# Kernel optimization log

Hardware: AMD Instinct MI355X
Metric: run time of the kernel (lower is better)

The kernel has to match this reference:

```python
import jax, jax.numpy as jnp
import numpy as np

N, E = 50000, 800000
IN_DIM, H, OUT = 16, 256, 64
L = 3
REL_DIM, ROLE_DIM, COL_DIM = 16, 8, 8
NUM_REL, NUM_ROLE, NUM_COL = 8, 8, 3
EDGE_IN = 2 * H + REL_DIM + 2 * ROLE_DIM + 2 * COL_DIM   # 560
NODE_IN = 2 * H + ROLE_DIM + COL_DIM                     # 528
LN_EPS = 1e-5


def setup_inputs() -> dict:
    key = jax.random.key(0)
    ks = jax.random.split(key, 32)
    s = 0.02
    inp = {
        "scalars": jax.random.normal(ks[0], (N, IN_DIM), jnp.float32),
        "edge_index": jax.random.randint(ks[1], (2, E), 0, N),
        "edge_relation": jax.random.randint(ks[2], (E,), 0, NUM_REL),
        "node_color_rep": jax.random.randint(ks[3], (N,), 0, NUM_COL),
        "node_role": jax.random.randint(ks[4], (N,), 0, NUM_ROLE),
        # block-level embeddings + input projection (weights stored [in,out])
        "blk_role_emb": jax.random.normal(ks[5], (NUM_ROLE, 8), jnp.float32) * s,
        "blk_color_emb": jax.random.normal(ks[6], (NUM_COL, 8), jnp.float32) * s,
        "in_w": jax.random.normal(ks[7], (IN_DIM + 16, H), jnp.float32) * s,
        "in_b": jnp.zeros((H,), jnp.float32),
        # per-layer params, stacked over L
        "rel_embs": jax.random.normal(ks[8], (L, NUM_REL, REL_DIM), jnp.float32) * s,
        "role_embs": jax.random.normal(ks[9], (L, NUM_ROLE, ROLE_DIM), jnp.float32) * s,
        "col_embs": jax.random.normal(ks[10], (L, NUM_COL, COL_DIM), jnp.float32) * s,
        "e1_w": jax.random.normal(ks[11], (L, EDGE_IN, H), jnp.float32) * s,
        "e1_b": jnp.zeros((L, H), jnp.float32),
        "e2_w": jax.random.normal(ks[12], (L, H, H), jnp.float32) * s,
        "e2_b": jnp.zeros((L, H), jnp.float32),
        "n1_w": jax.random.normal(ks[13], (L, NODE_IN, H), jnp.float32) * s,
        "n1_b": jnp.zeros((L, H), jnp.float32),
        "n2_w": jax.random.normal(ks[14], (L, H, H), jnp.float32) * s,
        "n2_b": jnp.zeros((L, H), jnp.float32),
        "ln_g": jnp.ones((L, H), jnp.float32),
        "ln_b": jnp.zeros((L, H), jnp.float32),
        "out_w": jax.random.normal(ks[15], (H, OUT), jnp.float32) * s,
        "out_b": jnp.zeros((OUT,), jnp.float32),
    }
    return inp


def _layer(h, edge_index, edge_relation, node_color_rep, node_role,
           rel_e, role_e, col_e, e1w, e1b, e2w, e2b, n1w, n1b, n2w, n2b, g, b):
    src, dst = edge_index[0], edge_index[1]
    role_all = role_e[node_role]           # [N, ROLE_DIM]
    col_all = col_e[node_color_rep]        # [N, COL_DIM]
    edge_in = jnp.concatenate(
        [h[src], h[dst], rel_e[edge_relation],
         role_all[src], role_all[dst], col_all[src], col_all[dst]], axis=-1)
    m = jax.nn.silu(edge_in @ e1w + e1b)
    m = jax.nn.silu(m @ e2w + e2b)                       # [E, H]
    agg = jax.ops.segment_sum(m, dst, num_segments=h.shape[0])
    node_in = jnp.concatenate([h, agg, role_all, col_all], axis=-1)
    upd = jax.nn.silu(node_in @ n1w + n1b) @ n2w + n2b
    x = h + upd
    mu = jnp.mean(x, axis=-1, keepdims=True)
    var = jnp.mean(jnp.square(x - mu), axis=-1, keepdims=True)
    return g * (x - mu) * jax.lax.rsqrt(var + LN_EPS) + b


def reference(scalars, edge_index, edge_relation, node_color_rep, node_role,
              blk_role_emb, blk_color_emb, in_w, in_b,
              rel_embs, role_embs, col_embs,
              e1_w, e1_b, e2_w, e2_b, n1_w, n1_b, n2_w, n2_b,
              ln_g, ln_b, out_w, out_b):
    node_in = jnp.concatenate(
        [scalars, blk_color_emb[node_color_rep], blk_role_emb[node_role]], axis=-1)
    h = node_in @ in_w + in_b
    for i in range(L):
        h = _layer(h, edge_index, edge_relation, node_color_rep, node_role,
                   rel_embs[i], role_embs[i], col_embs[i],
                   e1_w[i], e1_b[i], e2_w[i], e2_b[i],
                   n1_w[i], n1_b[i], n2_w[i], n2_b[i],
                   ln_g[i], ln_b[i])
    return h @ out_w + out_b
```

## Files before the change

### kernel.cpp

```cpp
#include <hip/hip_runtime.h>

#define NN 50000
#define NE 800000
#define H 256
#define NB (NE / 64)
#define NBINS 50176

typedef __bf16 bf16x8 __attribute__((ext_vector_type(8)));
typedef __bf16 bf16x4 __attribute__((ext_vector_type(4)));
typedef float f32x4 __attribute__((ext_vector_type(4)));

static __device__ __forceinline__ f32x4 mfma16(bf16x8 a, bf16x8 b, f32x4 c) {
  return __builtin_amdgcn_mfma_f32_16x16x32_bf16(a, b, c, 0, 0, 0);
}
static __device__ __forceinline__ bf16x8 bzero8() {
  bf16x8 z;
#pragma unroll
  for (int j = 0; j < 8; ++j) z[j] = (__bf16)0.f;
  return z;
}
static __device__ __forceinline__ float silu_f(float v) {
  return v * __builtin_amdgcn_rcpf(1.f + __builtin_amdgcn_exp2f(v * -1.442695041f));
}
static __device__ __forceinline__ void add4(float4& a, const float4 b) {
  a.x += b.x; a.y += b.y; a.z += b.z; a.w += b.w;
}

__global__ void prep_kernel(
    const float* __restrict__ e1w, const float* __restrict__ e2w,
    const float* __restrict__ n1w, const float* __restrict__ n2w,
    const float* __restrict__ outw, const float* __restrict__ e1b,
    const float* __restrict__ rel_embs, const float* __restrict__ role_embs,
    const float* __restrict__ col_embs,
    __bf16* __restrict__ wsd, __bf16* __restrict__ e2p,
    __bf16* __restrict__ n1p, __bf16* __restrict__ n2p,
    __bf16* __restrict__ outp, int* __restrict__ cnt,
    float* __restrict__ TR, float* __restrict__ TS, float* __restrict__ TD)
{
  int i = blockIdx.x * 256 + threadIdx.x;
  if (i < 3 * 131072) {
    const int l = i / 131072, rem = i % 131072;
    const int c = rem >> 14, r2 = rem & 16383;
    const int n = r2 >> 5, k = c * 32 + (r2 & 31);
    wsd[i] = (n < 256) ? (__bf16)e1w[((size_t)l * 560 + k) * 256 + n]
                       : (__bf16)e1w[((size_t)l * 560 + 256 + k) * 256 + (n - 256)];
    return;
  }
  i -= 3 * 131072;
  if (i < 3 * 65536) {
    const int l = i / 65536, rem = i % 65536;
    const int c = rem >> 13, r2 = rem & 8191;
    const int n = r2 >> 5, k = c * 32 + (r2 & 31);
    e2p[i] = (__bf16)e2w[((size_t)l * 256 + k) * 256 + n];
    return;
  }
  i -= 3 * 65536;
  if (i < 3 * 139264) {
    const int l = i / 139264, rem = i % 139264;
    const int c = rem >> 13, r2 = rem & 8191;
    const int n = r2 >> 5, k = c * 32 + (r2 & 31);
    n1p[i] = (k < 528) ? (__bf16)n1w[((size_t)l * 528 + k) * 256 + n] : (__bf16)0.f;
    return;
  }
  i -= 3 * 139264;
  if (i < 3 * 65536) {
    const int l = i / 65536, rem = i % 65536;
    const int c = rem >> 13, r2 = rem & 8191;
    const int n = r2 >> 5, k = c * 32 + (r2 & 31);
    n2p[i] = (__bf16)n2w[((size_t)l * 256 + k) * 256 + n];
    return;
  }
  i -= 3 * 65536;
  if (i < 16384) {
    const int c = i >> 11, r2 = i & 2047;
    const int n = r2 >> 5, k = c * 32 + (r2 & 31);
    outp[i] = (__bf16)outw[(size_t)k * 64 + n];
    return;
  }
  i -= 16384;
  if (i < NBINS) { cnt[i] = 0; return; }
  i -= NBINS;
  if (i < 768) {
    const int l = i >> 8, c = i & 255;
    float w[48];
#pragma unroll
    for (int j = 0; j < 48; ++j) w[j] = e1w[((size_t)l * 560 + 512 + j) * 256 + c];
#pragma unroll
    for (int r = 0; r < 8; ++r) {
      float s = 0.f;
#pragma unroll
      for (int j = 0; j < 16; ++j) s += rel_embs[l * 128 + r * 16 + j] * w[j];
      TR[((size_t)l * 8 + r) * 256 + c] = s;
    }
    const float bias = e1b[l * 256 + c];
#pragma unroll
    for (int ro = 0; ro < 8; ++ro) {
      float ss = 0.f, sd = 0.f;
#pragma unroll
      for (int j = 0; j < 8; ++j) {
        ss += role_embs[l * 64 + ro * 8 + j] * w[16 + j];
        sd += role_embs[l * 64 + ro * 8 + j] * w[24 + j];
      }
#pragma unroll
      for (int co = 0; co < 3; ++co) {
        float cs = 0.f, cd = 0.f;
#pragma unroll
        for (int j = 0; j < 8; ++j) {
          cs += col_embs[l * 24 + co * 8 + j] * w[32 + j];
          cd += col_embs[l * 24 + co * 8 + j] * w[40 + j];
        }
        TS[((size_t)l * 24 + ro * 3 + co) * 256 + c] = ss + cs;
        TD[((size_t)l * 24 + ro * 3 + co) * 256 + c] = sd + cd + bias;
      }
    }
  }
}

__global__ void hist_kernel(const int* __restrict__ dstI, int* __restrict__ cnt) {
  const int e = blockIdx.x * 256 + threadIdx.x;
  if (e < NE) atomicAdd(&cnt[dstI[e]], 1);
}

__global__ __launch_bounds__(1024) void scan_kernel(int* __restrict__ cnt) {
  __shared__ int wsum[16];
  __shared__ int carry;
  const int tid = threadIdx.x, lane = tid & 63, wid = tid >> 6;
  if (tid == 0) carry = 0;
  __syncthreads();
  for (int base = 0; base < NBINS; base += 4096) {
    const int idx = base + tid * 4;
    int4 v = make_int4(0, 0, 0, 0);
    if (idx < NBINS) v = *(const int4*)&cnt[idx];
    const int s1 = v.x + v.y, s2 = s1 + v.z, tot = s2 + v.w;
    int x = tot;
#pragma unroll
    for (int d = 1; d < 64; d <<= 1) {
      const int y = __shfl_up(x, d, 64);
      if (lane >= d) x += y;
    }
    if (lane == 63) wsum[wid] = x;
    __syncthreads();
    int wpref = 0;
#pragma unroll
    for (int w = 0; w < 16; ++w)
      if (w < wid) wpref += wsum[w];
    const int ex = carry + wpref + (x - tot);
    if (idx < NBINS) {
      int4 o;
      o.x = ex; o.y = ex + v.x; o.z = ex + s1; o.w = ex + s2;
      *(int4*)&cnt[idx] = o;
    }
    __syncthreads();
    if (tid == 0) {
      int s = 0;
#pragma unroll
      for (int w = 0; w < 16; ++w) s += wsum[w];
      carry += s;
    }
    __syncthreads();
  }
}

__global__ void scatter_kernel(const int* __restrict__ srcI, const int* __restrict__ dstI,
                               const int* __restrict__ erel, int* __restrict__ cnt,
                               int* __restrict__ esr, int* __restrict__ dstS) {
  const int e = blockIdx.x * 256 + threadIdx.x;
  if (e < NE) {
    const int d = dstI[e];
    const int pos = atomicAdd(&cnt[d], 1);
    esr[pos] = srcI[e] | (erel[e] << 16);
    dstS[pos] = d;
  }
}

__global__ __launch_bounds__(256) void embed_kernel(
    const float* __restrict__ scalars, const int* __restrict__ ncol,
    const int* __restrict__ nrole,
    const float* __restrict__ colEmb, const float* __restrict__ roleEmb,
    const float* __restrict__ inw, const float* __restrict__ inb,
    __bf16* __restrict__ h)
{
  __shared__ float sW[32][256];
  __shared__ float sIn[16][32];
  const int tid = threadIdx.x;
  const int n0 = blockIdx.x * 16;
#pragma unroll
  for (int j = 0; j < 32; ++j) sW[j][tid] = inw[j * 256 + tid];
  {
    const int node = tid >> 4, k = tid & 15;
    const int n = n0 + node;
    sIn[node][k] = (n < NN) ? scalars[(size_t)n * 16 + k] : 0.f;
  }
  if (tid < 16) {
    const int n = n0 + tid;
    if (n < NN) {
      const int c = ncol[n], r = nrole[n];
#pragma unroll
      for (int j = 0; j < 8; ++j) {
        sIn[tid][16 + j] = colEmb[c * 8 + j];
        sIn[tid][24 + j] = roleEmb[r * 8 + j];
      }
    } else {
#pragma unroll
      for (int j = 0; j < 16; ++j) sIn[tid][16 + j] = 0.f;
    }
  }
  __syncthreads();
  const float bias = inb[tid];
  for (int nn = 0; nn < 16; ++nn) {
    const int n = n0 + nn;
    if (n >= NN) break;
    float acc = bias;
#pragma unroll
    for (int k = 0; k < 32; ++k) acc += sIn[nn][k] * sW[k][tid];
    h[(size_t)n * H + tid] = (__bf16)acc;
  }
}

__global__ __launch_bounds__(256, 4) void pre_kernel(
    const __bf16* __restrict__ h, const int* __restrict__ nrole,
    const int* __restrict__ ncol, const __bf16* __restrict__ wsd,
    const float* __restrict__ TS, const float* __restrict__ TD,
    __bf16* __restrict__ PS, __bf16* __restrict__ PD)
{
  __shared__ __align__(16) __bf16 Ah[64][72];
  const int tid  = threadIdx.x;
  const int lane = tid & 63;
  const int wave = tid >> 6;
  const int l15  = lane & 15;
  const int quad = lane >> 4;
  const int n0   = (blockIdx.x >> 1) * 64;
  const int half = blockIdx.x & 1;
  const int colW = wave * 64;

  f32x4 acc[4][4] = {};
  for (int s = 0; s < 4; ++s) {
    if (s) __syncthreads();
#pragma unroll
    for (int it = 0; it < 2; ++it) {
      const int t = tid + it * 256;
      const int row = t >> 3, seg = t & 7;
      const int n = n0 + row;
      bf16x8 v = bzero8();
      if (n < NN) v = *(const bf16x8*)(h + (size_t)n * H + s * 64 + seg * 8);
      *(bf16x8*)&Ah[row][seg * 8] = v;
    }
    __syncthreads();
#pragma unroll
    for (int cc = 0; cc < 2; ++cc) {
      const int c = 2 * s + cc;
      bf16x8 bfr[4], afr[4];
#pragma unroll
      for (int nj = 0; nj < 4; ++nj)
        bfr[nj] = *(const bf16x8*)(wsd + ((size_t)c * 512 + half * 256 + colW + nj * 16 + l15) * 32 + quad * 8);
#pragma unroll
      for (int mi = 0; mi < 4; ++mi)
        afr[mi] = *(const bf16x8*)&Ah[mi * 16 + l15][cc * 32 + quad * 8];
#pragma unroll
      for (int mi = 0; mi < 4; ++mi)
#pragma unroll
        for (int nj = 0; nj < 4; ++nj)
          acc[mi][nj] = mfma16(afr[mi], bfr[nj], acc[mi][nj]);
    }
  }

  const float* T = half ? TD : TS;
  __bf16* P = half ? PD : PS;
#pragma unroll
  for (int mi = 0; mi < 4; ++mi)
#pragma unroll
    for (int r = 0; r < 4; ++r) {
      const int n = n0 + mi * 16 + quad * 4 + r;
      if (n < NN) {
        const int ti = (nrole[n] * 3 + ncol[n]) * 256;
#pragma unroll
        for (int nj = 0; nj < 4; ++nj) {
          const int col = colW + nj * 16 + l15;
          P[(size_t)n * H + col] = (__bf16)(acc[mi][nj][r] + T[ti + col]);
        }
      }
    }
}

__global__ __launch_bounds__(256, 4) void edge_kernel(
    const __bf16* __restrict__ PS, const __bf16* __restrict__ PD,
    float* __restrict__ agg, float* __restrict__ bnd,
    const int* __restrict__ esr, const int* __restrict__ dstS,
    const float* __restrict__ TR,
    const __bf16* __restrict__ e2p, const float* __restrict__ e2b)
{
  __shared__ __align__(16) char uni[34816];
  __shared__ __bf16 sTrel[8][256];
  __shared__ int sSrc[64], sDst[64], sRel[64];

  auto A2  = (__bf16 (*)[264])uni;
  auto A2t = (__bf16 (*)[68])uni;

  const int tid  = threadIdx.x;
  const int lane = tid & 63;
  const int wave = tid >> 6;
  const int l15  = lane & 15;
  const int quad = lane >> 4;
  const int e0   = blockIdx.x * 64;
  const int colW = wave * 64;

  if (tid < 64) {
    const int u = esr[e0 + tid];
    sSrc[tid] = u & 0xffff;
    sRel[tid] = u >> 16;
    sDst[tid] = dstS[e0 + tid];
  }
  {
    const int r = tid >> 5, cs = (tid & 31) * 8;
    const float* p = TR + r * 256 + cs;
    bf16x8 v;
#pragma unroll
    for (int j = 0; j < 8; ++j) v[j] = (__bf16)p[j];
    *(bf16x8*)&sTrel[r][cs] = v;
  }
  __syncthreads();

  {
    const int brow = tid >> 5;
    const int cs = (tid & 31) * 8;
#pragma unroll
    for (int it = 0; it < 8; ++it) {
      const int row = it * 8 + brow;
      const bf16x8 a = *(const bf16x8*)(PS + (size_t)sSrc[row] * H + cs);
      const bf16x8 b = *(const bf16x8*)(PD + (size_t)sDst[row] * H + cs);
      const bf16x8 t = *(const bf16x8*)&sTrel[sRel[row]][cs];
      bf16x8 o;
#pragma unroll
      for (int j = 0; j < 8; ++j)
        o[j] = (__bf16)silu_f((float)a[j] + (float)b[j] + (float)t[j]);
      *(bf16x8*)&A2[row][cs] = o;
    }
  }
  __syncthreads();

  f32x4 acc2[4][4] = {};
#pragma unroll
  for (int c = 0; c < 8; ++c) {
    bf16x8 bfr[4], afr[4];
#pragma unroll
    for (int nj = 0; nj < 4; ++nj)
      bfr[nj] = *(const bf16x8*)(e2p + ((size_t)c * 256 + colW + nj * 16 + l15) * 32 + quad * 8);
#pragma unroll
    for (int mi = 0; mi < 4; ++mi)
      afr[mi] = *(const bf16x8*)&A2[mi * 16 + l15][c * 32 + quad * 8];
#pragma unroll
    for (int mi = 0; mi < 4; ++mi)
#pragma unroll
      for (int nj = 0; nj < 4; ++nj)
        acc2[mi][nj] = mfma16(afr[mi], bfr[nj], acc2[mi][nj]);
  }

  float b2[4];
#pragma unroll
  for (int nj = 0; nj < 4; ++nj) b2[nj] = e2b[colW + nj * 16 + l15];
  __syncthreads();

#pragma unroll
  for (int mi = 0; mi < 4; ++mi)
#pragma unroll
    for (int nj = 0; nj < 4; ++nj) {
      const int col = colW + nj * 16 + l15;
      bf16x4 pv;
#pragma unroll
      for (int r = 0; r < 4; ++r)
        pv[r] = (__bf16)silu_f(acc2[mi][nj][r] + b2[nj]);
      *(bf16x4*)&A2t[col][mi * 16 + quad * 4] = pv;
    }
  __syncthreads();

  {
    const int col = tid;
    const bool f = (lane > 0) && (sDst[lane] != sDst[lane - 1]);
    const unsigned long long mask = __ballot(f);
    bf16x4 v[16];
#pragma unroll
    for (int j = 0; j < 16; ++j) v[j] = *(const bf16x4*)&A2t[col][j * 4];
    float* bnd0 = bnd + ((size_t)2 * blockIdx.x) * 256 + col;
    float sum = 0.f;
    int s0 = 0;
#pragma unroll
    for (int r = 0; r < 64; ++r) {
      sum += (float)v[r >> 2][r & 3];
      if (r == 63 || ((mask >> (r + 1)) & 1ull)) {
        const bool isFirst = (s0 == 0), isLast = (r == 63);
        if (isFirst) {
          bnd0[0] = isLast ? 0.f : sum;
          if (isLast) bnd0[256] = sum;
        } else if (isLast) {
          bnd0[256] = sum;
        } else {
          agg[(size_t)sDst[r] * H + col] = sum;
        }
        sum = 0.f;
        s0 = r + 1;
      }
    }
  }
}

__global__ __launch_bounds__(256, 4) void node_kernel(
    __bf16* __restrict__ h, const float* __restrict__ agg,
    const float* __restrict__ bnd, const int* __restrict__ cnt,
    const int* __restrict__ nrole, const int* __restrict__ ncol,
    const float* __restrict__ roleE, const float* __restrict__ colE,
    const __bf16* __restrict__ n1p, const float* __restrict__ n1b,
    const __bf16* __restrict__ n2p, const float* __restrict__ n2b,
    const float* __restrict__ lng, const float* __restrict__ lnb,
    const int mode,
    const __bf16* __restrict__ wsdN, const float* __restrict__ TSn,
    const float* __restrict__ TDn, __bf16* __restrict__ PS, __bf16* __restrict__ PD,
    const __bf16* __restrict__ outp, const float* __restrict__ outb,
    float* __restrict__ out)
{
  __shared__ __align__(16) char uni[33792];
  __shared__ __bf16 sRole[8][8], sCol[3][8];
  __shared__ float sSum[64][4], sSsq[64][4];
  __shared__ int sStart[64], sEnd[64], sTi[64];

  auto Abuf = (__bf16 (*)[72])uni;
  auto A2   = (__bf16 (*)[264])uni;

  const int tid  = threadIdx.x;
  const int lane = tid & 63;
  const int wave = tid >> 6;
  const int l15  = lane & 15;
  const int quad = lane >> 4;
  const int n0   = blockIdx.x * 64;
  const int colW = wave * 64;

  if (tid < 64) {
    const int n = n0 + tid;
    int st = 0, en = 0, ti = 0;
    if (n < NN) {
      st = (n > 0) ? cnt[n - 1] : 0;
      en = cnt[n];
      ti = (nrole[n] * 3 + ncol[n]) * 256;
    }
    sStart[tid] = st; sEnd[tid] = en; sTi[tid] = ti;
    ((__bf16*)sRole)[tid] = (__bf16)roleE[tid];
  } else if (tid < 88) {
    ((__bf16*)sCol)[tid - 64] = (__bf16)colE[tid - 64];
  }
  __syncthreads();

  f32x4 acc[4][4] = {};
  for (int s = 0; s < 9; ++s) {
    if (s) __syncthreads();
    if (s < 4) {
#pragma unroll
      for (int it = 0; it < 2; ++it) {
        const int t = tid + it * 256;
        const int row = t >> 3, seg = t & 7;
        const int n = n0 + row;
        bf16x8 v = bzero8();
        if (n < NN) v = *(const bf16x8*)(h + (size_t)n * H + s * 64 + seg * 8);
        *(bf16x8*)&Abuf[row][seg * 8] = v;
      }
    } else if (s < 8) {
#pragma unroll
      for (int it = 0; it < 2; ++it) {
        const int t = tid + it * 256;
        const int row = t >> 3, seg = t & 7;
        const int off = (s - 4) * 64 + seg * 8;
        const int st = sStart[row], en = sEnd[row];
        float4 u0 = make_float4(0.f, 0.f, 0.f, 0.f);
        float4 u1 = make_float4(0.f, 0.f, 0.f, 0.f);
        if (en > st) {
          const int bs = st >> 6, be = (en - 1) >> 6;
          const bool interior = (bs == be) && (st & 63) != 0 && (en & 63) != 0;
          if (interior) {
            const float* p = agg + (size_t)(n0 + row) * H + off;
            u0 = *(const float4*)p;
            u1 = *(const float4*)(p + 4);
          } else {
            for (int b = bs; b <= be; ++b) {
              if (b > bs || (st & 63) == 0) {
                const float* p = bnd + ((size_t)2 * b) * 256 + off;
                add4(u0, *(const float4*)p);
                add4(u1, *(const float4*)(p + 4));
              }
              if (b < be || (en & 63) == 0) {
                const float* p = bnd + ((size_t)2 * b + 1) * 256 + off;
                add4(u0, *(const float4*)p);
                add4(u1, *(const float4*)(p + 4));
              }
            }
          }
        }
        bf16x8 v;
        v[0] = (__bf16)u0.x; v[1] = (__bf16)u0.y; v[2] = (__bf16)u0.z; v[3] = (__bf16)u0.w;
        v[4] = (__bf16)u1.x; v[5] = (__bf16)u1.y; v[6] = (__bf16)u1.z; v[7] = (__bf16)u1.w;
        *(bf16x8*)&Abuf[row][seg * 8] = v;
      }
    } else {
      const int row = tid >> 2, q = tid & 3;
      const int n = n0 + row;
      __bf16* dp = &Abuf[row][q * 16];
      if (q == 0 && n < NN) {
        const int r = nrole[n], c = ncol[n];
#pragma unroll
        for (int j = 0; j < 8; ++j) { dp[j] = sRole[r][j]; dp[8 + j] = sCol[c][j]; }
      } else {
#pragma unroll
        for (int j = 0; j < 16; ++j) dp[j] = (__bf16)0.f;
      }
    }
    __syncthreads();
#pragma unroll
    for (int cc = 0; cc < 2; ++cc) {
      const int c = 2 * s + cc;
      if (c >= 17) break;
      bf16x8 bfr[4], afr[4];
#pragma unroll
      for (int nj = 0; nj < 4; ++nj)
        bfr[nj] = *(const bf16x8*)(n1p + ((size_t)c * 256 + colW + nj * 16 + l15) * 32 + quad * 8);
#pragma unroll
      for (int mi = 0; mi < 4; ++mi)
        afr[mi] = *(const bf16x8*)&Abuf[mi * 16 + l15][cc * 32 + quad * 8];
#pragma unroll
      for (int mi = 0; mi < 4; ++mi)
#pragma unroll
        for (int nj = 0; nj < 4; ++nj)
          acc[mi][nj] = mfma16(afr[mi], bfr[nj], acc[mi][nj]);
    }
  }
  __syncthreads();

  float b1[4];
#pragma unroll
  for (int nj = 0; nj < 4; ++nj) b1[nj] = n1b[colW + nj * 16 + l15];
#pragma unroll
  for (int mi = 0; mi < 4; ++mi)
#pragma unroll
    for (int nj = 0; nj < 4; ++nj)
#pragma unroll
      for (int r = 0; r < 4; ++r)
        A2[mi * 16 + quad * 4 + r][colW + nj * 16 + l15] =
            (__bf16)silu_f(acc[mi][nj][r] + b1[nj]);
  __syncthreads();

  f32x4 acc2[4][4] = {};
#pragma unroll
  for (int c = 0; c < 8; ++c) {
    bf16x8 bfr[4], afr[4];
#pragma unroll
    for (int nj = 0; nj < 4; ++nj)
      bfr[nj] = *(const bf16x8*)(n2p + ((size_t)c * 256 + colW + nj * 16 + l15) * 32 + quad * 8);
#pragma unroll
    for (int mi = 0; mi < 4; ++mi)
      afr[mi] = *(const bf16x8*)&A2[mi * 16 + l15][c * 32 + quad * 8];
#pragma unroll
    for (int mi = 0; mi < 4; ++mi)
#pragma unroll
      for (int nj = 0; nj < 4; ++nj)
        acc2[mi][nj] = mfma16(afr[mi], bfr[nj], acc2[mi][nj]);
  }

  float b2[4], g4[4], bb4[4];
#pragma unroll
  for (int nj = 0; nj < 4; ++nj) {
    const int col = colW + nj * 16 + l15;
    b2[nj] = n2b[col]; g4[nj] = lng[col]; bb4[nj] = lnb[col];
  }
#pragma unroll
  for (int mi = 0; mi < 4; ++mi)
#pragma unroll
    for (int r = 0; r < 4; ++r) {
      const int n = n0 + mi * 16 + quad * 4 + r;
#pragma unroll
      for (int nj = 0; nj < 4; ++nj) {
        const float hv = (n < NN) ? (float)h[(size_t)n * H + colW + nj * 16 + l15] : 0.f;
        acc2[mi][nj][r] += b2[nj] + hv;
      }
    }
#pragma unroll
  for (int mi = 0; mi < 4; ++mi)
#pragma unroll
    for (int r = 0; r < 4; ++r) {
      float s1 = 0.f, s2 = 0.f;
#pragma unroll
      for (int nj = 0; nj < 4; ++nj) {
        const float v = acc2[mi][nj][r];
        s1 += v; s2 += v * v;
      }
#pragma unroll
      for (int d = 1; d < 16; d <<= 1) {
        s1 += __shfl_xor(s1, d, 16);
        s2 += __shfl_xor(s2, d, 16);
      }
      if (l15 == 0) {
        const int row = mi * 16 + quad * 4 + r;
        sSum[row][wave] = s1; sSsq[row][wave] = s2;
      }
    }
  __syncthreads();

#pragma unroll
  for (int mi = 0; mi < 4; ++mi)
#pragma unroll
    for (int r = 0; r < 4; ++r) {
      const int row = mi * 16 + quad * 4 + r;
      const int n = n0 + row;
      const float t1 = sSum[row][0] + sSum[row][1] + sSum[row][2] + sSum[row][3];
      const float t2 = sSsq[row][0] + sSsq[row][1] + sSsq[row][2] + sSsq[row][3];
      const float mu = t1 * (1.f / 256.f);
      float var = t2 * (1.f / 256.f) - mu * mu;
      var = var < 0.f ? 0.f : var;
      const float rstd = rsqrtf(var + 1e-5f);
#pragma unroll
      for (int nj = 0; nj < 4; ++nj) {
        const int col = colW + nj * 16 + l15;
        const float o = g4[nj] * (acc2[mi][nj][r] - mu) * rstd + bb4[nj];
        const __bf16 ob = (__bf16)o;
        A2[row][col] = ob;
        if (mode == 0 && n < NN) h[(size_t)n * H + col] = ob;
      }
    }
  __syncthreads();

  if (mode == 0) {
    for (int hf = 0; hf < 2; ++hf) {
      f32x4 ap[4][4] = {};
#pragma unroll
      for (int c = 0; c < 8; ++c) {
        bf16x8 bfr[4], afr[4];
#pragma unroll
        for (int nj = 0; nj < 4; ++nj)
          bfr[nj] = *(const bf16x8*)(wsdN + ((size_t)c * 512 + hf * 256 + colW + nj * 16 + l15) * 32 + quad * 8);
#pragma unroll
        for (int mi = 0; mi < 4; ++mi)
          afr[mi] = *(const bf16x8*)&A2[mi * 16 + l15][c * 32 + quad * 8];
#pragma unroll
        for (int mi = 0; mi < 4; ++mi)
#pragma unroll
          for (int nj = 0; nj < 4; ++nj)
            ap[mi][nj] = mfma16(afr[mi], bfr[nj], ap[mi][nj]);
      }
      const float* T = hf ? TDn : TSn;
      __bf16* P = hf ? PD : PS;
#pragma unroll
      for (int mi = 0; mi < 4; ++mi)
#pragma unroll
        for (int r = 0; r < 4; ++r) {
          const int row = mi * 16 + quad * 4 + r;
          const int n = n0 + row;
          if (n < NN) {
            const int ti = sTi[row];
#pragma unroll
            for (int nj = 0; nj < 4; ++nj) {
              const int col = colW + nj * 16 + l15;
              P[(size_t)n * H + col] = (__bf16)(ap[mi][nj][r] + T[ti + col]);
            }
          }
        }
    }
  } else {
    f32x4 ao[4] = {};
#pragma unroll
    for (int c = 0; c < 8; ++c) {
      const bf16x8 bfr = *(const bf16x8*)(outp + ((size_t)c * 64 + wave * 16 + l15) * 32 + quad * 8);
#pragma unroll
      for (int mi = 0; mi < 4; ++mi) {
        const bf16x8 afr = *(const bf16x8*)&A2[mi * 16 + l15][c * 32 + quad * 8];
        ao[mi] = mfma16(afr, bfr, ao[mi]);
      }
    }
    const float ob = outb[wave * 16 + l15];
#pragma unroll
    for (int mi = 0; mi < 4; ++mi)
#pragma unroll
      for (int r = 0; r < 4; ++r) {
        const int n = n0 + mi * 16 + quad * 4 + r;
        if (n < NN) out[(size_t)n * 64 + wave * 16 + l15] = ao[mi][r] + ob;
      }
  }
}

extern "C" void kernel_launch(void* const* d_in, const int* in_sizes, int n_in,
                              void* d_out, int out_size, void* d_ws, size_t ws_size,
                              hipStream_t stream) {
  const float* scalars   = (const float*)d_in[0];
  const int*   ei        = (const int*)d_in[1];
  const int*   erel      = (const int*)d_in[2];
  const int*   ncol      = (const int*)d_in[3];
  const int*   nrole     = (const int*)d_in[4];
  const float* blk_role  = (const float*)d_in[5];
  const float* blk_col   = (const float*)d_in[6];
  const float* inw       = (const float*)d_in[7];
  const float* inb       = (const float*)d_in[8];
  const float* rel_embs  = (const float*)d_in[9];
  const float* role_embs = (const float*)d_in[10];
  const float* col_embs  = (const float*)d_in[11];
  const float* e1w       = (const float*)d_in[12];
  const float* e1b       = (const float*)d_in[13];
  const float* e2w       = (const float*)d_in[14];
  const float* e2b       = (const float*)d_in[15];
  const float* n1w       = (const float*)d_in[16];
  const float* n1b       = (const float*)d_in[17];
  const float* n2w       = (const float*)d_in[18];
  const float* n2b       = (const float*)d_in[19];
  const float* lng       = (const float*)d_in[20];
  const float* lnb       = (const float*)d_in[21];
  const float* outw      = (const float*)d_in[22];
  const float* outb      = (const float*)d_in[23];

  const int* srcI = ei;
  const int* dstI = ei + NE;

  char* ws = (char*)d_ws;
  size_t off = 0;
  auto take = [&](size_t bytes) -> char* {
    off = (off + 255) & ~(size_t)255;
    char* p = ws + off;
    off += bytes;
    return p;
  };
  __bf16* h    = (__bf16*)take((size_t)NN * H * 2);
  float*  agg  = (float*)take((size_t)NN * H * 4);
  float*  bnd  = (float*)take((size_t)2 * NB * 256 * 4);
  __bf16* PS   = (__bf16*)take((size_t)NN * H * 2);
  __bf16* PD   = (__bf16*)take((size_t)NN * H * 2);
  __bf16* wsd  = (__bf16*)take((size_t)3 * 131072 * 2);
  __bf16* e2p  = (__bf16*)take((size_t)3 * 65536 * 2);
  __bf16* n1p  = (__bf16*)take((size_t)3 * 139264 * 2);
  __bf16* n2p  = (__bf16*)take((size_t)3 * 65536 * 2);
  __bf16* outp = (__bf16*)take((size_t)16384 * 2);
  float*  TR   = (float*)take((size_t)3 * 8 * 256 * 4);
  float*  TS   = (float*)take((size_t)3 * 24 * 256 * 4);
  float*  TD   = (float*)take((size_t)3 * 24 * 256 * 4);
  int*    cnt  = (int*)take((size_t)NBINS * 4);
  int*    esr  = (int*)take((size_t)NE * 4);
  int*    dstS = (int*)take((size_t)NE * 4);

  prep_kernel<<<4967, 256, 0, stream>>>(e1w, e2w, n1w, n2w, outw, e1b,
                                        rel_embs, role_embs, col_embs,
                                        wsd, e2p, n1p, n2p, outp, cnt, TR, TS, TD);
  hist_kernel<<<(NE + 255) / 256, 256, 0, stream>>>(dstI, cnt);
  scan_kernel<<<1, 1024, 0, stream>>>(cnt);
  scatter_kernel<<<(NE + 255) / 256, 256, 0, stream>>>(srcI, dstI, erel, cnt,
                                                       esr, dstS);
  embed_kernel<<<(NN + 15) / 16, 256, 0, stream>>>(scalars, ncol, nrole,
                                                   blk_col, blk_role, inw, inb, h);
  pre_kernel<<<2 * ((NN + 63) / 64), 256, 0, stream>>>(
      h, nrole, ncol, wsd, TS, TD, PS, PD);

  for (int l = 0; l < 3; ++l) {
    edge_kernel<<<NB, 256, 0, stream>>>(
        PS, PD, agg, bnd, esr, dstS, TR + (size_t)l * 2048,
        e2p + (size_t)l * 65536, e2b + (size_t)l * 256);
    const int mode = (l < 2) ? 0 : 1;
    node_kernel<<<(NN + 63) / 64, 256, 0, stream>>>(
        h, agg, bnd, cnt, nrole, ncol,
        role_embs + (size_t)l * 64, col_embs + (size_t)l * 24,
        n1p + (size_t)l * 139264, n1b + (size_t)l * 256,
        n2p + (size_t)l * 65536,  n2b + (size_t)l * 256,
        lng + (size_t)l * 256, lnb + (size_t)l * 256,
        mode,
        wsd + (size_t)(l + 1 < 3 ? l + 1 : 0) * 131072,
        TS + (size_t)(l + 1 < 3 ? l + 1 : 0) * 6144,
        TD + (size_t)(l + 1 < 3 ? l + 1 : 0) * 6144,
        PS, PD, outp, outb, (float*)d_out);
  }
}
```

Measured before the change: 1.308 ms.

## Merge setup kernels, fold node role/color embeddings into bias table, remap edge blocks

```diff
diff --git a/kernel.cpp b/kernel.cpp
--- a/kernel.cpp
+++ b/kernel.cpp
@@ -3,7 +3,7 @@
 #define NN 50000
 #define NE 800000
 #define H 256
-#define NB (NE / 64)
+#define NB 12500
 #define NBINS 50176
 
 typedef __bf16 bf16x8 __attribute__((ext_vector_type(8)));
@@ -26,17 +26,24 @@
   a.x += b.x; a.y += b.y; a.z += b.z; a.w += b.w;
 }
 
-__global__ void prep_kernel(
+__global__ void preph_kernel(
     const float* __restrict__ e1w, const float* __restrict__ e2w,
     const float* __restrict__ n1w, const float* __restrict__ n2w,
     const float* __restrict__ outw, const float* __restrict__ e1b,
+    const float* __restrict__ n1b,
     const float* __restrict__ rel_embs, const float* __restrict__ role_embs,
-    const float* __restrict__ col_embs,
+    const float* __restrict__ col_embs, const int* __restrict__ dstI,
     __bf16* __restrict__ wsd, __bf16* __restrict__ e2p,
     __bf16* __restrict__ n1p, __bf16* __restrict__ n2p,
     __bf16* __restrict__ outp, int* __restrict__ cnt,
-    float* __restrict__ TR, float* __restrict__ TS, float* __restrict__ TD)
+    float* __restrict__ TR, float* __restrict__ TS, float* __restrict__ TD,
+    float* __restrict__ TN)
 {
+  if (blockIdx.x >= 4675) {
+    const int e = (blockIdx.x - 4675) * 256 + threadIdx.x;
+    if (e < NE) atomicAdd(&cnt[dstI[e]], 1);
+    return;
+  }
   int i = blockIdx.x * 256 + threadIdx.x;
   if (i < 3 * 131072) {
     const int l = i / 131072, rem = i % 131072;
@@ -55,14 +62,14 @@
     return;
   }
   i -= 3 * 65536;
-  if (i < 3 * 139264) {
-    const int l = i / 139264, rem = i % 139264;
+  if (i < 3 * 131072) {
+    const int l = i / 131072, rem = i % 131072;
     const int c = rem >> 13, r2 = rem & 8191;
     const int n = r2 >> 5, k = c * 32 + (r2 & 31);
-    n1p[i] = (k < 528) ? (__bf16)n1w[((size_t)l * 528 + k) * 256 + n] : (__bf16)0.f;
+    n1p[i] = (__bf16)n1w[((size_t)l * 528 + k) * 256 + n];
     return;
   }
-  i -= 3 * 139264;
+  i -= 3 * 131072;
   if (i < 3 * 65536) {
     const int l = i / 65536, rem = i % 65536;
     const int c = rem >> 13, r2 = rem & 8191;
@@ -78,8 +85,6 @@
     return;
   }
   i -= 16384;
-  if (i < NBINS) { cnt[i] = 0; return; }
-  i -= NBINS;
   if (i < 768) {
     const int l = i >> 8, c = i & 255;
     float w[48];
@@ -92,33 +97,38 @@
       for (int j = 0; j < 16; ++j) s += rel_embs[l * 128 + r * 16 + j] * w[j];
       TR[((size_t)l * 8 + r) * 256 + c] = s;
     }
+    float wn[16];
+#pragma unroll
+    for (int j = 0; j < 16; ++j) wn[j] = n1w[((size_t)l * 528 + 512 + j) * 256 + c];
     const float bias = e1b[l * 256 + c];
+    const float nbias = n1b[l * 256 + c];
 #pragma unroll
     for (int ro = 0; ro < 8; ++ro) {
-      float ss = 0.f, sd = 0.f;
+      float ss = 0.f, sd = 0.f, sn = 0.f;
 #pragma unroll
       for (int j = 0; j < 8; ++j) {
-        ss += role_embs[l * 64 + ro * 8 + j] * w[16 + j];
-        sd += role_embs[l * 64 + ro * 8 + j] * w[24 + j];
+        const float re = role_embs[l * 64 + ro * 8 + j];
+        ss += re * w[16 + j];
+        sd += re * w[24 + j];
+        sn += re * wn[j];
       }
 #pragma unroll
       for (int co = 0; co < 3; ++co) {
-        float cs = 0.f, cd = 0.f;
+        float cs = 0.f, cd = 0.f, cn = 0.f;
 #pragma unroll
         for (int j = 0; j < 8; ++j) {
-          cs += col_embs[l * 24 + co * 8 + j] * w[32 + j];
-          cd += col_embs[l * 24 + co * 8 + j] * w[40 + j];
+          const float ce = col_embs[l * 24 + co * 8 + j];
+          cs += ce * w[32 + j];
+          cd += ce * w[40 + j];
+          cn += ce * wn[8 + j];
         }
-        TS[((size_t)l * 24 + ro * 3 + co) * 256 + c] = ss + cs;
-        TD[((size_t)l * 24 + ro * 3 + co) * 256 + c] = sd + cd + bias;
-      }
-    }
-  }
-}
-
-__global__ void hist_kernel(const int* __restrict__ dstI, int* __restrict__ cnt) {
-  const int e = blockIdx.x * 256 + threadIdx.x;
-  if (e < NE) atomicAdd(&cnt[dstI[e]], 1);
+        const size_t o = ((size_t)l * 24 + ro * 3 + co) * 256 + c;
+        TS[o] = ss + cs;
+        TD[o] = sd + cd + bias;
+        TN[o] = sn + cn + nbias;
+      }
+    }
+  }
 }
 
 __global__ __launch_bounds__(1024) void scan_kernel(int* __restrict__ cnt) {
@@ -161,125 +171,143 @@
   }
 }
 
-__global__ void scatter_kernel(const int* __restrict__ srcI, const int* __restrict__ dstI,
-                               const int* __restrict__ erel, int* __restrict__ cnt,
-                               int* __restrict__ esr, int* __restrict__ dstS) {
-  const int e = blockIdx.x * 256 + threadIdx.x;
-  if (e < NE) {
-    const int d = dstI[e];
-    const int pos = atomicAdd(&cnt[d], 1);
-    esr[pos] = srcI[e] | (erel[e] << 16);
-    dstS[pos] = d;
-  }
-}
-
-__global__ __launch_bounds__(256) void embed_kernel(
+__global__ __launch_bounds__(256, 4) void scem_kernel(
+    const int* __restrict__ srcI, const int* __restrict__ dstI,
+    const int* __restrict__ erel, int* __restrict__ cnt,
+    int* __restrict__ esr, int* __restrict__ dstS,
     const float* __restrict__ scalars, const int* __restrict__ ncol,
     const int* __restrict__ nrole,
     const float* __restrict__ colEmb, const float* __restrict__ roleEmb,
     const float* __restrict__ inw, const float* __restrict__ inb,
-    __bf16* __restrict__ h)
+    const __bf16* __restrict__ wsd,
+    const float* __restrict__ TS, const float* __restrict__ TD,
+    __bf16* __restrict__ h, __bf16* __restrict__ PS, __bf16* __restrict__ PD)
 {
-  __shared__ float sW[32][256];
-  __shared__ float sIn[16][32];
-  const int tid = threadIdx.x;
-  const int n0 = blockIdx.x * 16;
-#pragma unroll
-  for (int j = 0; j < 32; ++j) sW[j][tid] = inw[j * 256 + tid];
-  {
-    const int node = tid >> 4, k = tid & 15;
-    const int n = n0 + node;
-    sIn[node][k] = (n < NN) ? scalars[(size_t)n * 16 + k] : 0.f;
-  }
-  if (tid < 16) {
-    const int n = n0 + tid;
-    if (n < NN) {
-      const int c = ncol[n], r = nrole[n];
-#pragma unroll
-      for (int j = 0; j < 8; ++j) {
-        sIn[tid][16 + j] = colEmb[c * 8 + j];
-        sIn[tid][24 + j] = roleEmb[r * 8 + j];
-      }
-    } else {
-#pragma unroll
-      for (int j = 0; j < 16; ++j) sIn[tid][16 + j] = 0.f;
-    }
-  }
-  __syncthreads();
-  const float bias = inb[tid];
-  for (int nn = 0; nn < 16; ++nn) {
-    const int n = n0 + nn;
-    if (n >= NN) break;
-    float acc = bias;
-#pragma unroll
-    for (int k = 0; k < 32; ++k) acc += sIn[nn][k] * sW[k][tid];
-    h[(size_t)n * H + tid] = (__bf16)acc;
-  }
-}
-
-__global__ __launch_bounds__(256, 4) void pre_kernel(
-    const __bf16* __restrict__ h, const int* __restrict__ nrole,
-    const int* __restrict__ ncol, const __bf16* __restrict__ wsd,
-    const float* __restrict__ TS, const float* __restrict__ TD,
-    __bf16* __restrict__ PS, __bf16* __restrict__ PD)
-{
-  __shared__ __align__(16) __bf16 Ah[64][72];
+  if (blockIdx.x < 3125) {
+    const int e = blockIdx.x * 256 + threadIdx.x;
+    if (e < NE) {
+      const int d = dstI[e];
+      const int pos = atomicAdd(&cnt[d], 1);
+      esr[pos] = srcI[e] | (erel[e] << 16);
+      dstS[pos] = d;
+    }
+    return;
+  }
+  __shared__ __align__(16) char uni[34816];
+  __shared__ int sTi[64];
+  auto Ain = (__bf16 (*)[40])uni;
+  auto Hs  = (__bf16 (*)[264])uni;
+
   const int tid  = threadIdx.x;
   const int lane = tid & 63;
   const int wave = tid >> 6;
   const int l15  = lane & 15;
   const int quad = lane >> 4;
-  const int n0   = (blockIdx.x >> 1) * 64;
-  const int half = blockIdx.x & 1;
+  const int n0   = (blockIdx.x - 3125) * 64;
   const int colW = wave * 64;
 
+  if (tid < 64) {
+    const int n = n0 + tid;
+    sTi[tid] = (n < NN) ? (nrole[n] * 3 + ncol[n]) * 256 : 0;
+  }
+  {
+    const int row = tid >> 2, q = tid & 3;
+    const int n = n0 + row;
+    __bf16* dp = &Ain[row][q * 8];
+    if (n < NN) {
+      if (q < 2) {
+#pragma unroll
+        for (int j = 0; j < 8; ++j) dp[j] = (__bf16)scalars[(size_t)n * 16 + q * 8 + j];
+      } else if (q == 2) {
+        const int c = ncol[n];
+#pragma unroll
+        for (int j = 0; j < 8; ++j) dp[j] = (__bf16)colEmb[c * 8 + j];
+      } else {
+        const int r = nrole[n];
+#pragma unroll
+        for (int j = 0; j < 8; ++j) dp[j] = (__bf16)roleEmb[r * 8 + j];
+      }
+    } else {
+#pragma unroll
+      for (int j = 0; j < 8; ++j) dp[j] = (__bf16)0.f;
+    }
+  }
+  __syncthreads();
+
   f32x4 acc[4][4] = {};
-  for (int s = 0; s < 4; ++s) {
-    if (s) __syncthreads();
-#pragma unroll
-    for (int it = 0; it < 2; ++it) {
-      const int t = tid + it * 256;
-      const int row = t >> 3, seg = t & 7;
+  {
+    bf16x8 bfr[4], afr[4];
+#pragma unroll
+    for (int nj = 0; nj < 4; ++nj) {
+      const int col = colW + nj * 16 + l15;
+#pragma unroll
+      for (int j = 0; j < 8; ++j) bfr[nj][j] = (__bf16)inw[(quad * 8 + j) * 256 + col];
+    }
+#pragma unroll
+    for (int mi = 0; mi < 4; ++mi)
+      afr[mi] = *(const bf16x8*)&Ain[mi * 16 + l15][quad * 8];
+#pragma unroll
+    for (int mi = 0; mi < 4; ++mi)
+#pragma unroll
+      for (int nj = 0; nj < 4; ++nj)
+        acc[mi][nj] = mfma16(afr[mi], bfr[nj], acc[mi][nj]);
+  }
+  float bi[4];
+#pragma unroll
+  for (int nj = 0; nj < 4; ++nj) bi[nj] = inb[colW + nj * 16 + l15];
+  __syncthreads();
+
+#pragma unroll
+  for (int mi = 0; mi < 4; ++mi)
+#pragma unroll
+    for (int r = 0; r < 4; ++r) {
+      const int row = mi * 16 + quad * 4 + r;
       const int n = n0 + row;
-      bf16x8 v = bzero8();
-      if (n < NN) v = *(const bf16x8*)(h + (size_t)n * H + s * 64 + seg * 8);
-      *(bf16x8*)&Ah[row][seg * 8] = v;
-    }
-    __syncthreads();
-#pragma unroll
-    for (int cc = 0; cc < 2; ++cc) {
-      const int c = 2 * s + cc;
+#pragma unroll
+      for (int nj = 0; nj < 4; ++nj) {
+        const int col = colW + nj * 16 + l15;
+        const __bf16 hv = (__bf16)(acc[mi][nj][r] + bi[nj]);
+        Hs[row][col] = hv;
+        if (n < NN) h[(size_t)n * H + col] = hv;
+      }
+    }
+  __syncthreads();
+
+  for (int hf = 0; hf < 2; ++hf) {
+    f32x4 ap[4][4] = {};
+#pragma unroll
+    for (int c = 0; c < 8; ++c) {
       bf16x8 bfr[4], afr[4];
 #pragma unroll
       for (int nj = 0; nj < 4; ++nj)
-        bfr[nj] = *(const bf16x8*)(wsd + ((size_t)c * 512 + half * 256 + colW + nj * 16 + l15) * 32 + quad * 8);
+        bfr[nj] = *(const bf16x8*)(wsd + ((size_t)c * 512 + hf * 256 + colW + nj * 16 + l15) * 32 + quad * 8);
 #pragma unroll
       for (int mi = 0; mi < 4; ++mi)
-        afr[mi] = *(const bf16x8*)&Ah[mi * 16 + l15][cc * 32 + quad * 8];
+        afr[mi] = *(const bf16x8*)&Hs[mi * 16 + l15][c * 32 + quad * 8];
 #pragma unroll
       for (int mi = 0; mi < 4; ++mi)
 #pragma unroll
         for (int nj = 0; nj < 4; ++nj)
-          acc[mi][nj] = mfma16(afr[mi], bfr[nj], acc[mi][nj]);
-    }
-  }
-
-  const float* T = half ? TD : TS;
-  __bf16* P = half ? PD : PS;
-#pragma unroll
-  for (int mi = 0; mi < 4; ++mi)
-#pragma unroll
-    for (int r = 0; r < 4; ++r) {
-      const int n = n0 + mi * 16 + quad * 4 + r;
-      if (n < NN) {
-        const int ti = (nrole[n] * 3 + ncol[n]) * 256;
-#pragma unroll
-        for (int nj = 0; nj < 4; ++nj) {
-          const int col = colW + nj * 16 + l15;
-          P[(size_t)n * H + col] = (__bf16)(acc[mi][nj][r] + T[ti + col]);
+          ap[mi][nj] = mfma16(afr[mi], bfr[nj], ap[mi][nj]);
+    }
+    const float* T = hf ? TD : TS;
+    __bf16* P = hf ? PD : PS;
+#pragma unroll
+    for (int mi = 0; mi < 4; ++mi)
+#pragma unroll
+      for (int r = 0; r < 4; ++r) {
+        const int row = mi * 16 + quad * 4 + r;
+        const int n = n0 + row;
+        if (n < NN) {
+          const int ti = sTi[row];
+#pragma unroll
+          for (int nj = 0; nj < 4; ++nj) {
+            const int col = colW + nj * 16 + l15;
+            P[(size_t)n * H + col] = (__bf16)(ap[mi][nj][r] + T[ti + col]);
+          }
         }
       }
-    }
+  }
 }
 
 __global__ __launch_bounds__(256, 4) void edge_kernel(
@@ -289,6 +317,10 @@
     const float* __restrict__ TR,
     const __bf16* __restrict__ e2p, const float* __restrict__ e2b)
 {
+  const int g = blockIdx.x;
+  const int bb = (g & 7) * 1563 + (g >> 3);
+  if (bb >= NB) return;
+
   __shared__ __align__(16) char uni[34816];
   __shared__ __bf16 sTrel[8][256];
   __shared__ int sSrc[64], sDst[64], sRel[64];
@@ -301,7 +333,7 @@
   const int wave = tid >> 6;
   const int l15  = lane & 15;
   const int quad = lane >> 4;
-  const int e0   = blockIdx.x * 64;
+  const int e0   = bb * 64;
   const int colW = wave * 64;
 
   if (tid < 64) {
@@ -380,7 +412,7 @@
     bf16x4 v[16];
 #pragma unroll
     for (int j = 0; j < 16; ++j) v[j] = *(const bf16x4*)&A2t[col][j * 4];
-    float* bnd0 = bnd + ((size_t)2 * blockIdx.x) * 256 + col;
+    float* bnd0 = bnd + ((size_t)2 * bb) * 256 + col;
     float sum = 0.f;
     int s0 = 0;
 #pragma unroll
@@ -407,8 +439,7 @@
     __bf16* __restrict__ h, const float* __restrict__ agg,
     const float* __restrict__ bnd, const int* __restrict__ cnt,
     const int* __restrict__ nrole, const int* __restrict__ ncol,
-    const float* __restrict__ roleE, const float* __restrict__ colE,
-    const __bf16* __restrict__ n1p, const float* __restrict__ n1b,
+    const __bf16* __restrict__ n1p, const float* __restrict__ TN,
     const __bf16* __restrict__ n2p, const float* __restrict__ n2b,
     const float* __restrict__ lng, const float* __restrict__ lnb,
     const int mode,
@@ -418,9 +449,8 @@
     float* __restrict__ out)
 {
   __shared__ __align__(16) char uni[33792];
-  __shared__ __bf16 sRole[8][8], sCol[3][8];
   __shared__ float sSum[64][4], sSsq[64][4];
-  __shared__ int sStart[64], sEnd[64], sTi[64];
+  __shared__ int sTi[64], sPcnt[64], sPidx[64][4];
 
   auto Abuf = (__bf16 (*)[72])uni;
   auto A2   = (__bf16 (*)[264])uni;
@@ -441,15 +471,27 @@
       en = cnt[n];
       ti = (nrole[n] * 3 + ncol[n]) * 256;
     }
-    sStart[tid] = st; sEnd[tid] = en; sTi[tid] = ti;
-    ((__bf16*)sRole)[tid] = (__bf16)roleE[tid];
-  } else if (tid < 88) {
-    ((__bf16*)sCol)[tid - 64] = (__bf16)colE[tid - 64];
+    sTi[tid] = ti;
+    int pc = 0, pidx[4] = {0, 0, 0, 0};
+    if (en > st) {
+      const int bs = st >> 6, be = (en - 1) >> 6;
+      if (bs == be && (st & 63) != 0 && (en & 63) != 0) {
+        pc = -1;
+      } else {
+        for (int b = bs; b <= be && pc < 4; ++b) {
+          if (b > bs || (st & 63) == 0) pidx[pc++] = 2 * b;
+          if ((b < be || (en & 63) == 0) && pc < 4) pidx[pc++] = 2 * b + 1;
+        }
+      }
+    }
+    sPcnt[tid] = pc;
+#pragma unroll
+    for (int j = 0; j < 4; ++j) sPidx[tid][j] = pidx[j];
   }
   __syncthreads();
 
   f32x4 acc[4][4] = {};
-  for (int s = 0; s < 9; ++s) {
+  for (int s = 0; s < 8; ++s) {
     if (s) __syncthreads();
     if (s < 4) {
 #pragma unroll
@@ -461,35 +503,24 @@
         if (n < NN) v = *(const bf16x8*)(h + (size_t)n * H + s * 64 + seg * 8);
         *(bf16x8*)&Abuf[row][seg * 8] = v;
       }
-    } else if (s < 8) {
+    } else {
 #pragma unroll
       for (int it = 0; it < 2; ++it) {
         const int t = tid + it * 256;
         const int row = t >> 3, seg = t & 7;
         const int off = (s - 4) * 64 + seg * 8;
-        const int st = sStart[row], en = sEnd[row];
+        const int pc = sPcnt[row];
         float4 u0 = make_float4(0.f, 0.f, 0.f, 0.f);
         float4 u1 = make_float4(0.f, 0.f, 0.f, 0.f);
-        if (en > st) {
-          const int bs = st >> 6, be = (en - 1) >> 6;
-          const bool interior = (bs == be) && (st & 63) != 0 && (en & 63) != 0;
-          if (interior) {
-            const float* p = agg + (size_t)(n0 + row) * H + off;
-            u0 = *(const float4*)p;
-            u1 = *(const float4*)(p + 4);
-          } else {
-            for (int b = bs; b <= be; ++b) {
-              if (b > bs || (st & 63) == 0) {
-                const float* p = bnd + ((size_t)2 * b) * 256 + off;
-                add4(u0, *(const float4*)p);
-                add4(u1, *(const float4*)(p + 4));
-              }
-              if (b < be || (en & 63) == 0) {
-                const float* p = bnd + ((size_t)2 * b + 1) * 256 + off;
-                add4(u0, *(const float4*)p);
-                add4(u1, *(const float4*)(p + 4));
-              }
-            }
+        if (pc == -1) {
+          const float* p = agg + (size_t)(n0 + row) * H + off;
+          u0 = *(const float4*)p;
+          u1 = *(const float4*)(p + 4);
+        } else {
+          for (int j = 0; j < pc; ++j) {
+            const float* p = bnd + (size_t)sPidx[row][j] * 256 + off;
+            add4(u0, *(const float4*)p);
+            add4(u1, *(const float4*)(p + 4));
           }
         }
         bf16x8 v;
@@ -497,24 +528,11 @@
         v[4] = (__bf16)u1.x; v[5] = (__bf16)u1.y; v[6] = (__bf16)u1.z; v[7] = (__bf16)u1.w;
         *(bf16x8*)&Abuf[row][seg * 8] = v;
       }
-    } else {
-      const int row = tid >> 2, q = tid & 3;
-      const int n = n0 + row;
-      __bf16* dp = &Abuf[row][q * 16];
-      if (q == 0 && n < NN) {
-        const int r = nrole[n], c = ncol[n];
-#pragma unroll
-        for (int j = 0; j < 8; ++j) { dp[j] = sRole[r][j]; dp[8 + j] = sCol[c][j]; }
-      } else {
-#pragma unroll
-        for (int j = 0; j < 16; ++j) dp[j] = (__bf16)0.f;
-      }
     }
     __syncthreads();
 #pragma unroll
     for (int cc = 0; cc < 2; ++cc) {
       const int c = 2 * s + cc;
-      if (c >= 17) break;
       bf16x8 bfr[4], afr[4];
 #pragma unroll
       for (int nj = 0; nj < 4; ++nj)
@@ -531,17 +549,18 @@
   }
   __syncthreads();
 
-  float b1[4];
-#pragma unroll
-  for (int nj = 0; nj < 4; ++nj) b1[nj] = n1b[colW + nj * 16 + l15];
 #pragma unroll
   for (int mi = 0; mi < 4; ++mi)
 #pragma unroll
-    for (int nj = 0; nj < 4; ++nj)
-#pragma unroll
-      for (int r = 0; r < 4; ++r)
-        A2[mi * 16 + quad * 4 + r][colW + nj * 16 + l15] =
-            (__bf16)silu_f(acc[mi][nj][r] + b1[nj]);
+    for (int r = 0; r < 4; ++r) {
+      const int row = mi * 16 + quad * 4 + r;
+      const int ti = sTi[row];
+#pragma unroll
+      for (int nj = 0; nj < 4; ++nj) {
+        const int col = colW + nj * 16 + l15;
+        A2[row][col] = (__bf16)silu_f(acc[mi][nj][r] + TN[ti + col]);
+      }
+    }
   __syncthreads();
 
   f32x4 acc2[4][4] = {};
@@ -727,43 +746,40 @@
   __bf16* PD   = (__bf16*)take((size_t)NN * H * 2);
   __bf16* wsd  = (__bf16*)take((size_t)3 * 131072 * 2);
   __bf16* e2p  = (__bf16*)take((size_t)3 * 65536 * 2);
-  __bf16* n1p  = (__bf16*)take((size_t)3 * 139264 * 2);
+  __bf16* n1p  = (__bf16*)take((size_t)3 * 131072 * 2);
   __bf16* n2p  = (__bf16*)take((size_t)3 * 65536 * 2);
   __bf16* outp = (__bf16*)take((size_t)16384 * 2);
   float*  TR   = (float*)take((size_t)3 * 8 * 256 * 4);
   float*  TS   = (float*)take((size_t)3 * 24 * 256 * 4);
   float*  TD   = (float*)take((size_t)3 * 24 * 256 * 4);
+  float*  TN   = (float*)take((size_t)3 * 24 * 256 * 4);
   int*    cnt  = (int*)take((size_t)NBINS * 4);
   int*    esr  = (int*)take((size_t)NE * 4);
   int*    dstS = (int*)take((size_t)NE * 4);
 
-  prep_kernel<<<4967, 256, 0, stream>>>(e1w, e2w, n1w, n2w, outw, e1b,
-                                        rel_embs, role_embs, col_embs,
-                                        wsd, e2p, n1p, n2p, outp, cnt, TR, TS, TD);
-  hist_kernel<<<(NE + 255) / 256, 256, 0, stream>>>(dstI, cnt);
+  hipMemsetAsync(cnt, 0, (size_t)NBINS * 4, stream);
+  preph_kernel<<<7800, 256, 0, stream>>>(
+      e1w, e2w, n1w, n2w, outw, e1b, n1b, rel_embs, role_embs, col_embs, dstI,
+      wsd, e2p, n1p, n2p, outp, cnt, TR, TS, TD, TN);
   scan_kernel<<<1, 1024, 0, stream>>>(cnt);
-  scatter_kernel<<<(NE + 255) / 256, 256, 0, stream>>>(srcI, dstI, erel, cnt,
-                                                       esr, dstS);
-  embed_kernel<<<(NN + 15) / 16, 256, 0, stream>>>(scalars, ncol, nrole,
-                                                   blk_col, blk_role, inw, inb, h);
-  pre_kernel<<<2 * ((NN + 63) / 64), 256, 0, stream>>>(
-      h, nrole, ncol, wsd, TS, TD, PS, PD);
+  scem_kernel<<<3907, 256, 0, stream>>>(
+      srcI, dstI, erel, cnt, esr, dstS,
+      scalars, ncol, nrole, blk_col, blk_role, inw, inb,
+      wsd, TS, TD, h, PS, PD);
 
   for (int l = 0; l < 3; ++l) {
-    edge_kernel<<<NB, 256, 0, stream>>>(
+    edge_kernel<<<12504, 256, 0, stream>>>(
         PS, PD, agg, bnd, esr, dstS, TR + (size_t)l * 2048,
         e2p + (size_t)l * 65536, e2b + (size_t)l * 256);
     const int mode = (l < 2) ? 0 : 1;
+    const int ln = (l + 1 < 3) ? l + 1 : 0;
     node_kernel<<<(NN + 63) / 64, 256, 0, stream>>>(
         h, agg, bnd, cnt, nrole, ncol,
-        role_embs + (size_t)l * 64, col_embs + (size_t)l * 24,
-        n1p + (size_t)l * 139264, n1b + (size_t)l * 256,
+        n1p + (size_t)l * 131072, TN + (size_t)l * 6144,
         n2p + (size_t)l * 65536,  n2b + (size_t)l * 256,
         lng + (size_t)l * 256, lnb + (size_t)l * 256,
         mode,
-        wsd + (size_t)(l + 1 < 3 ? l + 1 : 0) * 131072,
-        TS + (size_t)(l + 1 < 3 ? l + 1 : 0) * 6144,
-        TD + (size_t)(l + 1 < 3 ? l + 1 : 0) * 6144,
+        wsd + (size_t)ln * 131072, TS + (size_t)ln * 6144, TD + (size_t)ln * 6144,
         PS, PD, outp, outb, (float*)d_out);
   }
 }
```

After: 1.348 ms. 3.0% more time.
